# Performance work log

Hardware: AMD Instinct MI355X
Metric: run time of the kernel (lower is better)

Reference implementation:

```python
import jax, jax.numpy as jnp
import numpy as np

B, N, DIN, DOUT = 8, 2048, 64, 64
TAU = 2.0            # softmax temperature
NEG_SLOPE = 0.2      # LeakyReLU slope
EDGE_P = 0.02        # adjacency density


def setup_inputs() -> dict:
    key = jax.random.key(0)
    kx, ka, kw, ks, kd = jax.random.split(key, 5)
    x = jax.random.normal(kx, (B, N, DIN), dtype=jnp.float32)
    # sparse 0/1 road-graph adjacency with self-loops, stored dense as in the module
    A = (jax.random.uniform(ka, (B, N, N)) < EDGE_P).astype(jnp.float32)
    A = jnp.maximum(A, jnp.eye(N, dtype=jnp.float32)[None])
    # learned parameters (nn.Linear without bias): W [DIN,DOUT], a_src/a_dst [DOUT]
    W = jax.random.normal(kw, (DIN, DOUT), dtype=jnp.float32) / np.sqrt(DIN)
    a_src = jax.random.normal(ks, (DOUT,), dtype=jnp.float32) / np.sqrt(DOUT)
    a_dst = jax.random.normal(kd, (DOUT,), dtype=jnp.float32) / np.sqrt(DOUT)
    return {"x": x, "A": A, "W": W, "a_src": a_src, "a_dst": a_dst}


def reference(x, A, W, a_src, a_dst):
    Wx = jnp.einsum("bni,io->bno", x, W)          # [B,N,DOUT]
    e_src = jnp.einsum("bno,o->bn", Wx, a_src)     # [B,N]
    e_dst = jnp.einsum("bno,o->bn", Wx, a_dst)     # [B,N]
    e = e_src[:, :, None] + e_dst[:, None, :]      # [B,N,N]
    e = jnp.where(e > 0, e, NEG_SLOPE * e)         # LeakyReLU(0.2)
    e = jnp.where(A < 1e-9, -jnp.inf, e)           # mask non-edges
    alpha = jax.nn.softmax(e / TAU, axis=-1)
    alpha = jnp.nan_to_num(alpha, nan=0.0)         # rows with no neighbours -> 0
    return jnp.einsum("bnm,bmo->bno", alpha, Wx)   # [B,N,DOUT]
```

## Files before the change

kernel.cpp:

```cpp
#include <hip/hip_runtime.h>
#include <hip/hip_bf16.h>


#define BQ 8
#define NQ 2048
#define DQ 64
#define TAUQ 2.0f
#define SLOPEQ 0.2f
#define CAP 136

typedef float f4v __attribute__((ext_vector_type(4)));

__global__ __launch_bounds__(256) void gat_p1_scan(
    const float* __restrict__ x, const float* __restrict__ A,
    const float* __restrict__ W,
    const float* __restrict__ a_src, const float* __restrict__ a_dst,
    float* __restrict__ Wx, float* __restrict__ esrc, float* __restrict__ edst,
    unsigned* __restrict__ emask)
{
    const int t = threadIdx.x;
    const int wave = t >> 6, lane = t & 63;
    const int g = blockIdx.x;

    if (g % 3 == 2) {
        const int sidx = g / 3;
        const int r0 = sidx * 8 + wave * 2;
        const float* __restrict__ A0 = A + (size_t)r0 * NQ;
        f4v a[16];
#pragma unroll
        for (int k = 0; k < 16; ++k)
            a[k] = *reinterpret_cast<const f4v*>(A0 + k * 256 + 4 * lane);
        unsigned lm0 = 0, lm1 = 0;
#pragma unroll
        for (int k = 0; k < 8; ++k)
#pragma unroll
            for (int j = 0; j < 4; ++j) {
                if (a[k][j]     >= 1e-9f) lm0 |= 1u << (k * 4 + j);
                if (a[k + 8][j] >= 1e-9f) lm1 |= 1u << (k * 4 + j);
            }
        emask[(size_t)r0 * 64 + lane]       = lm0;
        emask[(size_t)(r0 + 1) * 64 + lane] = lm1;
        return;
    }

    const int pidx = (g / 3) * 2 + (g % 3);
    const int row = pidx * 4 + wave;

    __shared__ float Wl[64 * 64];
    __shared__ float xl[4][64];
    for (int i = t; i < 64 * 64; i += 256) Wl[i] = W[i];
    xl[wave][lane] = x[row * DQ + lane];
    __syncthreads();

    float acc = 0.f;
#pragma unroll
    for (int i = 0; i < 64; ++i)
        acc += xl[wave][i] * Wl[i * 64 + lane];
    Wx[row * DQ + lane] = acc;

    float ps = acc * a_src[lane];
    float pd = acc * a_dst[lane];
#pragma unroll
    for (int o = 32; o > 0; o >>= 1) {
        ps += __shfl_xor(ps, o);
        pd += __shfl_xor(pd, o);
    }
    if (lane == 0) { esrc[row] = ps; edst[row] = pd; }
}

__global__ __launch_bounds__(256) void gat_apply(
    const unsigned* __restrict__ emask, const float* __restrict__ Wx,
    const float* __restrict__ esrc, const float* __restrict__ edst,
    float* __restrict__ out)
{
    const int t = threadIdx.x;
    const int wave = t >> 6, lane = t & 63;
    const int row = blockIdx.x * 4 + wave;
    const int b = row >> 11;
    const float* __restrict__ ed = edst + b * NQ;
    const float  es = esrc[row];

    __shared__ int2 eL[4][CAP];

    unsigned lm = emask[(size_t)row * 64 + lane];

    const int cnt = __popc(lm);
    int incl = cnt;
#pragma unroll
    for (int o = 1; o < 64; o <<= 1) {
        int v = __shfl_up(incl, o);
        if (lane >= o) incl += v;
    }
    int total = __shfl(incl, 63);
    if (total > CAP - 8) total = CAP - 8;
    int base = incl - cnt;
    unsigned mrem = lm;
    while (mrem) {
        const int pos = __builtin_ctz(mrem);
        mrem &= mrem - 1;
        if (base < CAP - 8)
            eL[wave][base].x = ((pos >> 2) << 8) + 4 * lane + (pos & 3);
        ++base;
    }

    float mx = -INFINITY;
    for (int i = lane; i < total; i += 64) {
        const int m = eL[wave][i].x;
        float e = es + ed[m];
        e = e > 0.f ? e : SLOPEQ * e;
        eL[wave][i].y = __float_as_int(e);
        mx = fmaxf(mx, e);
    }
#pragma unroll
    for (int o = 32; o > 0; o >>= 1) mx = fmaxf(mx, __shfl_xor(mx, o));

    const float invtau = 1.0f / TAUQ;
    float s = 0.f;
    for (int i = lane; i < total; i += 64) {
        const float e = __int_as_float(eL[wave][i].y);
        const float p = __expf((e - mx) * invtau);
        eL[wave][i].y = __float_as_int(p);
        s += p;
    }
#pragma unroll
    for (int o = 32; o > 0; o >>= 1) s += __shfl_xor(s, o);
    const float inv = (s > 0.f) ? 1.0f / s : 0.f;

    const int pad = (8 - (total & 7)) & 7;
    if (lane < pad) eL[wave][total + lane] = make_int2(0, 0);
    const int padded = total + pad;

    const float* __restrict__ Wxb = Wx + (size_t)b * NQ * DQ;
    float acc = 0.f;
    for (int i = 0; i < padded; i += 8) {
        const int2 e0 = eL[wave][i + 0], e1 = eL[wave][i + 1];
        const int2 e2 = eL[wave][i + 2], e3 = eL[wave][i + 3];
        const int2 e4 = eL[wave][i + 4], e5 = eL[wave][i + 5];
        const int2 e6 = eL[wave][i + 6], e7 = eL[wave][i + 7];
        const float w0 = Wxb[((size_t)(unsigned)e0.x << 6) + lane];
        const float w1 = Wxb[((size_t)(unsigned)e1.x << 6) + lane];
        const float w2 = Wxb[((size_t)(unsigned)e2.x << 6) + lane];
        const float w3 = Wxb[((size_t)(unsigned)e3.x << 6) + lane];
        const float w4 = Wxb[((size_t)(unsigned)e4.x << 6) + lane];
        const float w5 = Wxb[((size_t)(unsigned)e5.x << 6) + lane];
        const float w6 = Wxb[((size_t)(unsigned)e6.x << 6) + lane];
        const float w7 = Wxb[((size_t)(unsigned)e7.x << 6) + lane];
        acc += __int_as_float(e0.y) * w0;
        acc += __int_as_float(e1.y) * w1;
        acc += __int_as_float(e2.y) * w2;
        acc += __int_as_float(e3.y) * w3;
        acc += __int_as_float(e4.y) * w4;
        acc += __int_as_float(e5.y) * w5;
        acc += __int_as_float(e6.y) * w6;
        acc += __int_as_float(e7.y) * w7;
    }
    out[(size_t)row * DQ + lane] = acc * inv;
}

extern "C" void kernel_launch(void* const* d_in, const int* in_sizes, int n_in,
                              void* d_out, int out_size, void* d_ws, size_t ws_size,
                              hipStream_t stream) {
    const float* x     = (const float*)d_in[0];
    const float* A     = (const float*)d_in[1];
    const float* W     = (const float*)d_in[2];
    const float* a_src = (const float*)d_in[3];
    const float* a_dst = (const float*)d_in[4];
    float* out = (float*)d_out;

    float*    Wx    = (float*)d_ws;
    float*    esrc  = Wx + (size_t)BQ * NQ * DQ;
    float*    edst  = esrc + (size_t)BQ * NQ;
    unsigned* emask = (unsigned*)(edst + (size_t)BQ * NQ);

    gat_p1_scan<<<6144, 256, 0, stream>>>(x, A, W, a_src, a_dst,
                                          Wx, esrc, edst, emask);
    gat_apply<<<BQ * NQ / 4, 256, 0, stream>>>(emask, Wx, esrc, edst, out);
}
```

Measured before the change: 43.01 us.

## Fuse projection and adjacency scan into one wave-per-two-rows streaming kernel

Replaces the heterogeneous block split (two projection blocks per scan block) with a single kernel where each wave handles two rows. It projects them through W held in registers, using readlane broadcasts instead of LDS, and bitmasks their adjacency rows. The A loads are issued before the matmul so memory latency overlaps compute, and the shared-memory W staging and barrier go away. The cost is a 64-float W copy per wave in registers, which raises register pressure, and every wave reloads W. The mask test also changes from >=1e-9 to !=0, which differs only for tiny or negative values.

```diff
diff --git a/kernel.cpp b/kernel.cpp
--- a/kernel.cpp
+++ b/kernel.cpp
@@ -11,7 +11,12 @@
 
 typedef float f4v __attribute__((ext_vector_type(4)));
 
-__global__ __launch_bounds__(256) void gat_p1_scan(
+__device__ __forceinline__ float bcast(float v, int i)
+{
+    return __int_as_float(__builtin_amdgcn_readlane(__float_as_int(v), i));
+}
+
+__global__ __launch_bounds__(256) void gat_stream(
     const float* __restrict__ x, const float* __restrict__ A,
     const float* __restrict__ W,
     const float* __restrict__ a_src, const float* __restrict__ a_dst,
@@ -20,52 +25,59 @@
 {
     const int t = threadIdx.x;
     const int wave = t >> 6, lane = t & 63;
-    const int g = blockIdx.x;
+    const int w = blockIdx.x * 4 + wave;
+    const int row0 = w * 2;
 
-    if (g % 3 == 2) {
-        const int sidx = g / 3;
-        const int r0 = sidx * 8 + wave * 2;
-        const float* __restrict__ A0 = A + (size_t)r0 * NQ;
-        f4v a[16];
+    float wreg[64];
 #pragma unroll
-        for (int k = 0; k < 16; ++k)
-            a[k] = *reinterpret_cast<const f4v*>(A0 + k * 256 + 4 * lane);
-        unsigned lm0 = 0, lm1 = 0;
+    for (int i = 0; i < 64; ++i)
+        wreg[i] = W[i * 64 + lane];
+    const float asr = a_src[lane], adr = a_dst[lane];
+    const float xv0 = x[(size_t)row0 * DQ + lane];
+    const float xv1 = x[((size_t)row0 + 1) * DQ + lane];
+
+    const float* __restrict__ Ar0 = A + (size_t)row0 * NQ;
+    f4v a0[8], a1[8];
 #pragma unroll
-        for (int k = 0; k < 8; ++k)
+    for (int k = 0; k < 8; ++k)
+        a0[k] = *reinterpret_cast<const f4v*>(Ar0 + k * 256 + 4 * lane);
 #pragma unroll
-            for (int j = 0; j < 4; ++j) {
-                if (a[k][j]     >= 1e-9f) lm0 |= 1u << (k * 4 + j);
-                if (a[k + 8][j] >= 1e-9f) lm1 |= 1u << (k * 4 + j);
-            }
-        emask[(size_t)r0 * 64 + lane]       = lm0;
-        emask[(size_t)(r0 + 1) * 64 + lane] = lm1;
-        return;
+    for (int k = 0; k < 8; ++k)
+        a1[k] = *reinterpret_cast<const f4v*>(Ar0 + NQ + k * 256 + 4 * lane);
+
+    float acc0 = 0.f, acc1 = 0.f;
+#pragma unroll
+    for (int i = 0; i < 64; ++i) {
+        acc0 = fmaf(bcast(xv0, i), wreg[i], acc0);
+        acc1 = fmaf(bcast(xv1, i), wreg[i], acc1);
+    }
+    Wx[(size_t)row0 * DQ + lane] = acc0;
+    Wx[((size_t)row0 + 1) * DQ + lane] = acc1;
+
+    float ps0 = acc0 * asr, pd0 = acc0 * adr;
+    float ps1 = acc1 * asr, pd1 = acc1 * adr;
+#pragma unroll
+    for (int o = 32; o > 0; o >>= 1) {
+        ps0 += __shfl_xor(ps0, o);
+        pd0 += __shfl_xor(pd0, o);
+        ps1 += __shfl_xor(ps1, o);
+        pd1 += __shfl_xor(pd1, o);
+    }
+    if (lane == 0) {
+        esrc[row0] = ps0; edst[row0] = pd0;
+        esrc[row0 + 1] = ps1; edst[row0 + 1] = pd1;
     }
 
-    const int pidx = (g / 3) * 2 + (g % 3);
-    const int row = pidx * 4 + wave;
-
-    __shared__ float Wl[64 * 64];
-    __shared__ float xl[4][64];
-    for (int i = t; i < 64 * 64; i += 256) Wl[i] = W[i];
-    xl[wave][lane] = x[row * DQ + lane];
-    __syncthreads();
-
-    float acc = 0.f;
+    unsigned lm0 = 0, lm1 = 0;
 #pragma unroll
-    for (int i = 0; i < 64; ++i)
-        acc += xl[wave][i] * Wl[i * 64 + lane];
-    Wx[row * DQ + lane] = acc;
-
-    float ps = acc * a_src[lane];
-    float pd = acc * a_dst[lane];
+    for (int k = 0; k < 8; ++k)
 #pragma unroll
-    for (int o = 32; o > 0; o >>= 1) {
-        ps += __shfl_xor(ps, o);
-        pd += __shfl_xor(pd, o);
-    }
-    if (lane == 0) { esrc[row] = ps; edst[row] = pd; }
+        for (int j = 0; j < 4; ++j) {
+            if (a0[k][j] != 0.f) lm0 |= 1u << (k * 4 + j);
+            if (a1[k][j] != 0.f) lm1 |= 1u << (k * 4 + j);
+        }
+    emask[(size_t)row0 * 64 + lane] = lm0;
+    emask[((size_t)row0 + 1) * 64 + lane] = lm1;
 }
 
 __global__ __launch_bounds__(256) void gat_apply(
@@ -172,7 +184,7 @@
     float*    edst  = esrc + (size_t)BQ * NQ;
     unsigned* emask = (unsigned*)(edst + (size_t)BQ * NQ);
 
-    gat_p1_scan<<<6144, 256, 0, stream>>>(x, A, W, a_src, a_dst,
-                                          Wx, esrc, edst, emask);
+    gat_stream<<<2048, 256, 0, stream>>>(x, A, W, a_src, a_dst,
+                                         Wx, esrc, edst, emask);
     gat_apply<<<BQ * NQ / 4, 256, 0, stream>>>(emask, Wx, esrc, edst, out);
 }
```

After: 42.34 us. About the same (-1.6%).

## Split adjacency scan across kernels to overlap with projection and apply

Applied to the files above, without the earlier changes.

The pipeline becomes three kernels. The first half of the adjacency-mask scan is interleaved with the Wx projection in kernel 1. The second half is interleaved with the apply of the first half of the rows in kernel 2, and kernel 3 applies the remaining rows. The aim is to overlap the memory-bound streaming of the dense adjacency with compute and gather work instead of front-loading it all. The inner gather loop also switches to a per-chunk fma chain and the mask test becomes != 0. These add a third launch and depend on the half-split row indexing staying consistent.

```diff
diff --git a/kernel.cpp b/kernel.cpp
--- a/kernel.cpp
+++ b/kernel.cpp
@@ -8,79 +8,42 @@
 #define TAUQ 2.0f
 #define SLOPEQ 0.2f
 #define CAP 136
+#define HALF (BQ * NQ / 2)
 
 typedef float f4v __attribute__((ext_vector_type(4)));
 
-__global__ __launch_bounds__(256) void gat_p1_scan(
-    const float* __restrict__ x, const float* __restrict__ A,
-    const float* __restrict__ W,
-    const float* __restrict__ a_src, const float* __restrict__ a_dst,
-    float* __restrict__ Wx, float* __restrict__ esrc, float* __restrict__ edst,
-    unsigned* __restrict__ emask)
-{
-    const int t = threadIdx.x;
-    const int wave = t >> 6, lane = t & 63;
-    const int g = blockIdx.x;
-
-    if (g % 3 == 2) {
-        const int sidx = g / 3;
-        const int r0 = sidx * 8 + wave * 2;
-        const float* __restrict__ A0 = A + (size_t)r0 * NQ;
-        f4v a[16];
-#pragma unroll
-        for (int k = 0; k < 16; ++k)
-            a[k] = *reinterpret_cast<const f4v*>(A0 + k * 256 + 4 * lane);
-        unsigned lm0 = 0, lm1 = 0;
-#pragma unroll
-        for (int k = 0; k < 8; ++k)
-#pragma unroll
-            for (int j = 0; j < 4; ++j) {
-                if (a[k][j]     >= 1e-9f) lm0 |= 1u << (k * 4 + j);
-                if (a[k + 8][j] >= 1e-9f) lm1 |= 1u << (k * 4 + j);
-            }
-        emask[(size_t)r0 * 64 + lane]       = lm0;
-        emask[(size_t)(r0 + 1) * 64 + lane] = lm1;
-        return;
-    }
-
-    const int pidx = (g / 3) * 2 + (g % 3);
-    const int row = pidx * 4 + wave;
-
-    __shared__ float Wl[64 * 64];
-    __shared__ float xl[4][64];
-    for (int i = t; i < 64 * 64; i += 256) Wl[i] = W[i];
-    xl[wave][lane] = x[row * DQ + lane];
-    __syncthreads();
-
-    float acc = 0.f;
-#pragma unroll
-    for (int i = 0; i < 64; ++i)
-        acc += xl[wave][i] * Wl[i * 64 + lane];
-    Wx[row * DQ + lane] = acc;
-
-    float ps = acc * a_src[lane];
-    float pd = acc * a_dst[lane];
-#pragma unroll
-    for (int o = 32; o > 0; o >>= 1) {
-        ps += __shfl_xor(ps, o);
-        pd += __shfl_xor(pd, o);
-    }
-    if (lane == 0) { esrc[row] = ps; edst[row] = pd; }
-}
-
-__global__ __launch_bounds__(256) void gat_apply(
+__device__ __forceinline__ void stream_rows(
+    const float* __restrict__ A, unsigned* __restrict__ emask, int row0, int lane)
+{
+    const float* __restrict__ Ar0 = A + (size_t)row0 * NQ;
+    f4v a0[8], a1[8];
+#pragma unroll
+    for (int k = 0; k < 8; ++k)
+        a0[k] = *reinterpret_cast<const f4v*>(Ar0 + k * 256 + 4 * lane);
+#pragma unroll
+    for (int k = 0; k < 8; ++k)
+        a1[k] = *reinterpret_cast<const f4v*>(Ar0 + NQ + k * 256 + 4 * lane);
+
+    unsigned lm0 = 0, lm1 = 0;
+#pragma unroll
+    for (int k = 0; k < 8; ++k)
+#pragma unroll
+        for (int j = 0; j < 4; ++j) {
+            if (a0[k][j] != 0.f) lm0 |= 1u << (k * 4 + j);
+            if (a1[k][j] != 0.f) lm1 |= 1u << (k * 4 + j);
+        }
+    emask[(size_t)row0 * 64 + lane] = lm0;
+    emask[((size_t)row0 + 1) * 64 + lane] = lm1;
+}
+
+__device__ __forceinline__ void apply_row(
     const unsigned* __restrict__ emask, const float* __restrict__ Wx,
     const float* __restrict__ esrc, const float* __restrict__ edst,
-    float* __restrict__ out)
-{
-    const int t = threadIdx.x;
-    const int wave = t >> 6, lane = t & 63;
-    const int row = blockIdx.x * 4 + wave;
+    float* __restrict__ out, int row, int wave, int lane, int2 (*eL)[CAP])
+{
     const int b = row >> 11;
     const float* __restrict__ ed = edst + b * NQ;
     const float  es = esrc[row];
-
-    __shared__ int2 eL[4][CAP];
 
     unsigned lm = emask[(size_t)row * 64 + lane];
 
@@ -145,16 +108,93 @@
         const float w5 = Wxb[((size_t)(unsigned)e5.x << 6) + lane];
         const float w6 = Wxb[((size_t)(unsigned)e6.x << 6) + lane];
         const float w7 = Wxb[((size_t)(unsigned)e7.x << 6) + lane];
-        acc += __int_as_float(e0.y) * w0;
-        acc += __int_as_float(e1.y) * w1;
-        acc += __int_as_float(e2.y) * w2;
-        acc += __int_as_float(e3.y) * w3;
-        acc += __int_as_float(e4.y) * w4;
-        acc += __int_as_float(e5.y) * w5;
-        acc += __int_as_float(e6.y) * w6;
-        acc += __int_as_float(e7.y) * w7;
+        float a = __int_as_float(e0.y) * w0;
+        a = fmaf(__int_as_float(e1.y), w1, a);
+        a = fmaf(__int_as_float(e2.y), w2, a);
+        a = fmaf(__int_as_float(e3.y), w3, a);
+        a = fmaf(__int_as_float(e4.y), w4, a);
+        a = fmaf(__int_as_float(e5.y), w5, a);
+        a = fmaf(__int_as_float(e6.y), w6, a);
+        a = fmaf(__int_as_float(e7.y), w7, a);
+        acc += a;
     }
     out[(size_t)row * DQ + lane] = acc * inv;
+}
+
+__global__ __launch_bounds__(256) void gat_k1(
+    const float* __restrict__ x, const float* __restrict__ A,
+    const float* __restrict__ W,
+    const float* __restrict__ a_src, const float* __restrict__ a_dst,
+    float* __restrict__ Wx, float* __restrict__ esrc, float* __restrict__ edst,
+    unsigned* __restrict__ emask)
+{
+    const int t = threadIdx.x;
+    const int wave = t >> 6, lane = t & 63;
+    const int g = blockIdx.x;
+
+    if (g % 5 == 0) {
+        const int w = (g / 5) * 4 + wave;
+        stream_rows(A, emask, w * 2, lane);
+        return;
+    }
+
+    const int p = (g / 5) * 4 + (g % 5) - 1;
+    const int row = p * 4 + wave;
+
+    __shared__ float Wl[64 * 64];
+    __shared__ float xl[4][64];
+    for (int i = t; i < 64 * 64; i += 256) Wl[i] = W[i];
+    xl[wave][lane] = x[(size_t)row * DQ + lane];
+    __syncthreads();
+
+    float acc = 0.f;
+#pragma unroll
+    for (int i = 0; i < 64; ++i)
+        acc += xl[wave][i] * Wl[i * 64 + lane];
+    Wx[(size_t)row * DQ + lane] = acc;
+
+    float ps = acc * a_src[lane];
+    float pd = acc * a_dst[lane];
+#pragma unroll
+    for (int o = 32; o > 0; o >>= 1) {
+        ps += __shfl_xor(ps, o);
+        pd += __shfl_xor(pd, o);
+    }
+    if (lane == 0) { esrc[row] = ps; edst[row] = pd; }
+}
+
+__global__ __launch_bounds__(256) void gat_k2(
+    const float* __restrict__ A, const unsigned* __restrict__ emask,
+    const float* __restrict__ Wx,
+    const float* __restrict__ esrc, const float* __restrict__ edst,
+    float* __restrict__ out, unsigned* __restrict__ emw)
+{
+    const int t = threadIdx.x;
+    const int wave = t >> 6, lane = t & 63;
+    const int g = blockIdx.x;
+
+    if (g % 3 == 0) {
+        const int w = (g / 3) * 4 + wave;
+        stream_rows(A, emw, HALF + w * 2, lane);
+        return;
+    }
+
+    __shared__ int2 eL[4][CAP];
+    const int a = (g / 3) * 2 + (g % 3) - 1;
+    const int row = a * 4 + wave;
+    apply_row(emask, Wx, esrc, edst, out, row, wave, lane, eL);
+}
+
+__global__ __launch_bounds__(256) void gat_k3(
+    const unsigned* __restrict__ emask, const float* __restrict__ Wx,
+    const float* __restrict__ esrc, const float* __restrict__ edst,
+    float* __restrict__ out)
+{
+    const int t = threadIdx.x;
+    const int wave = t >> 6, lane = t & 63;
+    __shared__ int2 eL[4][CAP];
+    const int row = HALF + blockIdx.x * 4 + wave;
+    apply_row(emask, Wx, esrc, edst, out, row, wave, lane, eL);
 }
 
 extern "C" void kernel_launch(void* const* d_in, const int* in_sizes, int n_in,
@@ -172,7 +212,8 @@
     float*    edst  = esrc + (size_t)BQ * NQ;
     unsigned* emask = (unsigned*)(edst + (size_t)BQ * NQ);
 
-    gat_p1_scan<<<6144, 256, 0, stream>>>(x, A, W, a_src, a_dst,
-                                          Wx, esrc, edst, emask);
-    gat_apply<<<BQ * NQ / 4, 256, 0, stream>>>(emask, Wx, esrc, edst, out);
-}
+    gat_k1<<<5120, 256, 0, stream>>>(x, A, W, a_src, a_dst,
+                                     Wx, esrc, edst, emask);
+    gat_k2<<<3072, 256, 0, stream>>>(A, emask, Wx, esrc, edst, out, emask);
+    gat_k3<<<2048, 256, 0, stream>>>(emask, Wx, esrc, edst, out);
+}
```

New measurement: 45.64 us. 6.1% more time.
